# Kernel optimization log

Hardware: AMD Instinct MI355X
Metric: run time of the kernel (lower is better)

Reference implementation:

```python
import jax, jax.numpy as jnp
import numpy as np


def _batch_conv2d(inputs, kernels):
    # inputs: [B, 1, H, W], kernels: [B, 1, 3, 3]; distinct kernel per sample
    # Implemented as a grouped conv: view inputs as [1, B, H, W], groups=B.
    B, _, H, W = inputs.shape
    out = jax.lax.conv_general_dilated(
        inputs.reshape(1, B, H, W),
        kernels,  # OIHW with O=B, I=1
        window_strides=(1, 1),
        padding=((1, 1), (1, 1)),
        feature_group_count=B,
        dimension_numbers=("NCHW", "OIHW", "NCHW"),
    )
    return out.reshape(B, 1, H, W)


def setup_inputs() -> dict:
    key = jax.random.key(0)
    k1, k2, k3 = jax.random.split(key, 3)
    B, m = 64, 512
    x = jax.random.normal(k1, (B, 1, m, m), dtype=jnp.float32)
    f = jax.random.normal(k2, (B, 1, m, m), dtype=jnp.float32)
    kernelA = jax.random.normal(k3, (B, 1, 3, 3), dtype=jnp.float32)
    return {"x": x, "f": f, "kernelA": kernelA}


def reference(x, f, kernelA):
    # One Jacobi-style smoothing step: x <- x + (f - A x) / 6
    Ax = _batch_conv2d(x, kernelA)
    x = x + (f - Ax) * (1.0 / 6.0)
    return x
```

## Files before the change

### kernel.cpp

```cpp
#include <hip/hip_runtime.h>

#define BB 64
#define HH 512
#define WW 512
#define RPT 2
#define ROWS_PER_BLOCK (4 * RPT)
#define NBLOCKS (BB * HH / ROWS_PER_BLOCK)

struct Q { float4 v; float l, r; };

__device__ __forceinline__ void accumq(float4& q, const Q& w,
                                       float w0, float w1, float w2) {
    q.x += w0 * w.l   + w1 * w.v.x + w2 * w.v.y;
    q.y += w0 * w.v.x + w1 * w.v.y + w2 * w.v.z;
    q.z += w0 * w.v.y + w1 * w.v.z + w2 * w.v.w;
    q.w += w0 * w.v.z + w1 * w.v.w + w2 * w.r;
}

__global__ __launch_bounds__(256) void jacobi_v8_kernel(
    const float* __restrict__ x,
    const float* __restrict__ f,
    const float* __restrict__ k,
    float* __restrict__ out)
{
    const int tid  = threadIdx.x;
    const int lane = tid & 63;
    const int wv   = tid >> 6;

    const int b  = blockIdx.x >> 6;
    const int rb = blockIdx.x & 63;
    const int r0 = (rb << 3) + wv * RPT;

    const size_t img = (size_t)b * (HH * WW);
    const float* xb = x + img;
    const float* fb = f + img;
    float*       ob = out + img;

    const float* kb = k + b * 9;
    const float k00 = kb[0], k01 = kb[1], k02 = kb[2];
    const float k10 = kb[3], k11 = kb[4], k12 = kb[5];
    const float k20 = kb[6], k21 = kb[7], k22 = kb[8];

    const int col = lane << 2;

    float4 xa[RPT + 2], xq[RPT + 2];
    #pragma unroll
    for (int t = 0; t < RPT + 2; ++t) {
        const int rr = r0 - 1 + t;
        if (rr >= 0 && rr < HH) {
            const float* p = xb + (size_t)rr * WW + col;
            xa[t] = *(const float4*)p;
            xq[t] = *(const float4*)(p + 256);
        } else {
            xa[t] = make_float4(0.f, 0.f, 0.f, 0.f);
            xq[t] = make_float4(0.f, 0.f, 0.f, 0.f);
        }
    }
    float4 fa[RPT], fq[RPT];
    #pragma unroll
    for (int r = 0; r < RPT; ++r) {
        const float* p = fb + (size_t)(r0 + r) * WW + col;
        fa[r] = *(const float4*)p;
        fq[r] = *(const float4*)(p + 256);
    }
    __builtin_amdgcn_sched_barrier(0);

    Q A[RPT + 2], B[RPT + 2];
    #pragma unroll
    for (int t = 0; t < RPT + 2; ++t) {
        const float a_l  = __shfl_up(xa[t].w, 1);
        const float a_r  = __shfl_down(xa[t].x, 1);
        const float b_l  = __shfl_up(xq[t].w, 1);
        const float b_r  = __shfl_down(xq[t].x, 1);
        const float aw63 = __shfl(xa[t].w, 63);
        const float bx0  = __shfl(xq[t].x, 0);
        A[t].v = xa[t];
        B[t].v = xq[t];
        A[t].l = (lane == 0)  ? 0.f  : a_l;
        A[t].r = (lane == 63) ? bx0  : a_r;
        B[t].l = (lane == 0)  ? aw63 : b_l;
        B[t].r = (lane == 63) ? 0.f  : b_r;
    }

    const float inv6 = 1.f / 6.f;
    #pragma unroll
    for (int r = 0; r < RPT; ++r) {
        float4 qa = make_float4(0.f, 0.f, 0.f, 0.f);
        float4 qb = make_float4(0.f, 0.f, 0.f, 0.f);
        accumq(qa, A[r],     k00, k01, k02);
        accumq(qa, A[r + 1], k10, k11, k12);
        accumq(qa, A[r + 2], k20, k21, k22);
        accumq(qb, B[r],     k00, k01, k02);
        accumq(qb, B[r + 1], k10, k11, k12);
        accumq(qb, B[r + 2], k20, k21, k22);

        const float4 ca = A[r + 1].v;
        const float4 cb = B[r + 1].v;
        float4 oa, obq;
        oa.x  = ca.x + (fa[r].x - qa.x) * inv6;
        oa.y  = ca.y + (fa[r].y - qa.y) * inv6;
        oa.z  = ca.z + (fa[r].z - qa.z) * inv6;
        oa.w  = ca.w + (fa[r].w - qa.w) * inv6;
        obq.x = cb.x + (fq[r].x - qb.x) * inv6;
        obq.y = cb.y + (fq[r].y - qb.y) * inv6;
        obq.z = cb.z + (fq[r].z - qb.z) * inv6;
        obq.w = cb.w + (fq[r].w - qb.w) * inv6;

        float* po = ob + (size_t)(r0 + r) * WW + col;
        *(float4*)po         = oa;
        *(float4*)(po + 256) = obq;
    }
}

extern "C" void kernel_launch(void* const* d_in, const int* in_sizes, int n_in,
                              void* d_out, int out_size, void* d_ws, size_t ws_size,
                              hipStream_t stream) {
    const float* x  = (const float*)d_in[0];
    const float* f  = (const float*)d_in[1];
    const float* kk = (const float*)d_in[2];
    float* out = (float*)d_out;

    jacobi_v8_kernel<<<NBLOCKS, 256, 0, stream>>>(x, f, kk, out);
}
```

Before: 170.5 us.

## Stage x tile with halo in shared memory to avoid redundant halo row loads

Each block now cooperatively loads its 8 output rows plus two halo rows of x into a shared-memory tile, then each wave reads its three stencil rows from LDS. This replaces per-wave global loads that re-fetched overlapping halo rows (16 row loads per block) with 10 row loads. It adds a block-wide barrier, LDS traffic, and 20 KB of shared memory per block, which may limit occupancy and add latency.

```diff
diff --git a/kernel.cpp b/kernel.cpp
--- a/kernel.cpp
+++ b/kernel.cpp
@@ -3,9 +3,8 @@
 #define BB 64
 #define HH 512
 #define WW 512
-#define RPT 2
-#define ROWS_PER_BLOCK (4 * RPT)
-#define NBLOCKS (BB * HH / ROWS_PER_BLOCK)
+#define TR 8
+#define NBLOCKS (BB * HH / TR)
 
 struct Q { float4 v; float l, r; };
 
@@ -17,19 +16,21 @@
     q.w += w0 * w.v.z + w1 * w.v.w + w2 * w.r;
 }
 
-__global__ __launch_bounds__(256) void jacobi_v8_kernel(
+__global__ __launch_bounds__(256) void jacobi_v10_kernel(
     const float* __restrict__ x,
     const float* __restrict__ f,
     const float* __restrict__ k,
     float* __restrict__ out)
 {
+    __shared__ float tile[(TR + 2) * WW];
+
     const int tid  = threadIdx.x;
     const int lane = tid & 63;
     const int wv   = tid >> 6;
 
     const int b  = blockIdx.x >> 6;
-    const int rb = blockIdx.x & 63;
-    const int r0 = (rb << 3) + wv * RPT;
+    const int tb = blockIdx.x & 63;
+    const int r0 = tb << 3;
 
     const size_t img = (size_t)b * (HH * WW);
     const float* xb = x + img;
@@ -43,72 +44,85 @@
 
     const int col = lane << 2;
 
-    float4 xa[RPT + 2], xq[RPT + 2];
+    float4 sv[5];
+    int    fl[5];
     #pragma unroll
-    for (int t = 0; t < RPT + 2; ++t) {
-        const int rr = r0 - 1 + t;
-        if (rr >= 0 && rr < HH) {
-            const float* p = xb + (size_t)rr * WW + col;
-            xa[t] = *(const float4*)p;
-            xq[t] = *(const float4*)(p + 256);
-        } else {
-            xa[t] = make_float4(0.f, 0.f, 0.f, 0.f);
-            xq[t] = make_float4(0.f, 0.f, 0.f, 0.f);
-        }
+    for (int s = 0; s < 5; ++s) {
+        const int flat = ((s << 8) + tid) << 2;
+        const int trow = flat >> 9;
+        const int tcol = flat & 511;
+        const int gr   = r0 - 1 + trow;
+        fl[s] = flat;
+        sv[s] = ((unsigned)gr < (unsigned)HH)
+                    ? *(const float4*)(xb + (size_t)gr * WW + tcol)
+                    : make_float4(0.f, 0.f, 0.f, 0.f);
     }
-    float4 fa[RPT], fq[RPT];
-    #pragma unroll
-    for (int r = 0; r < RPT; ++r) {
-        const float* p = fb + (size_t)(r0 + r) * WW + col;
-        fa[r] = *(const float4*)p;
-        fq[r] = *(const float4*)(p + 256);
-    }
+    const int i0 = r0 + (wv << 1);
+    const float* pf0 = fb + (size_t)i0 * WW + col;
+    const float* pf1 = pf0 + WW;
+    const float4 f0a = *(const float4*)pf0, f0b = *(const float4*)(pf0 + 256);
+    const float4 f1a = *(const float4*)pf1, f1b = *(const float4*)(pf1 + 256);
     __builtin_amdgcn_sched_barrier(0);
 
-    Q A[RPT + 2], B[RPT + 2];
     #pragma unroll
-    for (int t = 0; t < RPT + 2; ++t) {
-        const float a_l  = __shfl_up(xa[t].w, 1);
-        const float a_r  = __shfl_down(xa[t].x, 1);
-        const float b_l  = __shfl_up(xq[t].w, 1);
-        const float b_r  = __shfl_down(xq[t].x, 1);
-        const float aw63 = __shfl(xa[t].w, 63);
-        const float bx0  = __shfl(xq[t].x, 0);
-        A[t].v = xa[t];
-        B[t].v = xq[t];
-        A[t].l = (lane == 0)  ? 0.f  : a_l;
-        A[t].r = (lane == 63) ? bx0  : a_r;
-        B[t].l = (lane == 0)  ? aw63 : b_l;
-        B[t].r = (lane == 63) ? 0.f  : b_r;
-    }
+    for (int s = 0; s < 5; ++s)
+        *(float4*)(tile + fl[s]) = sv[s];
+    __syncthreads();
 
     const float inv6 = 1.f / 6.f;
     #pragma unroll
-    for (int r = 0; r < RPT; ++r) {
+    for (int j = 0; j < 2; ++j) {
+        const int orow = (wv << 1) + j;
+        float4 xa[3], xq[3];
+        #pragma unroll
+        for (int t = 0; t < 3; ++t) {
+            const float* lp = tile + (orow + t) * WW + col;
+            xa[t] = *(const float4*)lp;
+            xq[t] = *(const float4*)(lp + 256);
+        }
+        Q A[3], Bq[3];
+        #pragma unroll
+        for (int t = 0; t < 3; ++t) {
+            const float a_l  = __shfl_up(xa[t].w, 1);
+            const float a_r  = __shfl_down(xa[t].x, 1);
+            const float b_l  = __shfl_up(xq[t].w, 1);
+            const float b_r  = __shfl_down(xq[t].x, 1);
+            const float aw63 = __shfl(xa[t].w, 63);
+            const float bx0  = __shfl(xq[t].x, 0);
+            A[t].v  = xa[t];
+            Bq[t].v = xq[t];
+            A[t].l  = (lane == 0)  ? 0.f  : a_l;
+            A[t].r  = (lane == 63) ? bx0  : a_r;
+            Bq[t].l = (lane == 0)  ? aw63 : b_l;
+            Bq[t].r = (lane == 63) ? 0.f  : b_r;
+        }
+
         float4 qa = make_float4(0.f, 0.f, 0.f, 0.f);
         float4 qb = make_float4(0.f, 0.f, 0.f, 0.f);
-        accumq(qa, A[r],     k00, k01, k02);
-        accumq(qa, A[r + 1], k10, k11, k12);
-        accumq(qa, A[r + 2], k20, k21, k22);
-        accumq(qb, B[r],     k00, k01, k02);
-        accumq(qb, B[r + 1], k10, k11, k12);
-        accumq(qb, B[r + 2], k20, k21, k22);
+        accumq(qa, A[0],  k00, k01, k02);
+        accumq(qa, A[1],  k10, k11, k12);
+        accumq(qa, A[2],  k20, k21, k22);
+        accumq(qb, Bq[0], k00, k01, k02);
+        accumq(qb, Bq[1], k10, k11, k12);
+        accumq(qb, Bq[2], k20, k21, k22);
 
-        const float4 ca = A[r + 1].v;
-        const float4 cb = B[r + 1].v;
-        float4 oa, obq;
-        oa.x  = ca.x + (fa[r].x - qa.x) * inv6;
-        oa.y  = ca.y + (fa[r].y - qa.y) * inv6;
-        oa.z  = ca.z + (fa[r].z - qa.z) * inv6;
-        oa.w  = ca.w + (fa[r].w - qa.w) * inv6;
-        obq.x = cb.x + (fq[r].x - qb.x) * inv6;
-        obq.y = cb.y + (fq[r].y - qb.y) * inv6;
-        obq.z = cb.z + (fq[r].z - qb.z) * inv6;
-        obq.w = cb.w + (fq[r].w - qb.w) * inv6;
+        const float4 fa = j ? f1a : f0a;
+        const float4 fq = j ? f1b : f0b;
+        const float4 ca = A[1].v;
+        const float4 cb = Bq[1].v;
+        float4 oa, oq;
+        oa.x = ca.x + (fa.x - qa.x) * inv6;
+        oa.y = ca.y + (fa.y - qa.y) * inv6;
+        oa.z = ca.z + (fa.z - qa.z) * inv6;
+        oa.w = ca.w + (fa.w - qa.w) * inv6;
+        oq.x = cb.x + (fq.x - qb.x) * inv6;
+        oq.y = cb.y + (fq.y - qb.y) * inv6;
+        oq.z = cb.z + (fq.z - qb.z) * inv6;
+        oq.w = cb.w + (fq.w - qb.w) * inv6;
 
-        float* po = ob + (size_t)(r0 + r) * WW + col;
+        float* po = ob + (size_t)(i0 + j) * WW + col;
         *(float4*)po         = oa;
-        *(float4*)(po + 256) = obq;
+        *(float4*)(po + 256) = oq;
     }
 }
 
@@ -120,5 +134,5 @@
     const float* kk = (const float*)d_in[2];
     float* out = (float*)d_out;
 
-    jacobi_v8_kernel<<<NBLOCKS, 256, 0, stream>>>(x, f, kk, out);
+    jacobi_v10_kernel<<<NBLOCKS, 256, 0, stream>>>(x, f, kk, out);
 }
```

Measured after the change: 170.5 us. Within noise of the previous version (+0.0%).
